# Optimization experiments

Measured on AMD Instinct MI355X. Metric: run time of the kernel, lower is better.

## Reference

```python
import jax, jax.numpy as jnp
import numpy as np

B, D, H = 8, 512, 8
HD = D // H            # 64 head dim
NS, NT = 8192, 4096    # search / template points
ATTN_EPS = 1e-6
LN_EPS = 1e-5


def layer_norm(x, g, b):
    m = jnp.mean(x, axis=-1, keepdims=True)
    v = jnp.mean((x - m) ** 2, axis=-1, keepdims=True)
    return (x - m) * jax.lax.rsqrt(v + LN_EPS) * g + b


def setup_inputs() -> dict:
    key = jax.random.key(0)
    ks = jax.random.split(key, 20)
    s = 0.02
    return {
        "search_feat": jax.random.normal(ks[0], (B, D, NS), jnp.float32),
        "search_xyz": jax.random.uniform(ks[1], (B, NS, 3), jnp.float32),
        "template_feat": jax.random.normal(ks[2], (B, D, NT), jnp.float32),
        "template_xyz": jax.random.uniform(ks[3], (B, NT, 3), jnp.float32),
        "pos_w1": jax.random.normal(ks[4], (3, D), jnp.float32) * s,
        "pos_b1": jnp.zeros((D,), jnp.float32),
        "pos_w2": jax.random.normal(ks[5], (D, D), jnp.float32) * s,
        "pos_b2": jnp.zeros((D,), jnp.float32),
        "wq": jax.random.normal(ks[6], (D, D), jnp.float32) * s,
        "wk": jax.random.normal(ks[7], (D, D), jnp.float32) * s,
        "wv": jax.random.normal(ks[8], (D, D), jnp.float32) * s,
        "w_merge": jax.random.normal(ks[9], (D, D), jnp.float32) * s,
        "mlp_w1": jax.random.normal(ks[10], (2 * D, 2 * D), jnp.float32) * s,
        "mlp_w2": jax.random.normal(ks[11], (2 * D, D), jnp.float32) * s,
        "ln1_g": jnp.ones((D,), jnp.float32),
        "ln1_b": jnp.zeros((D,), jnp.float32),
        "ln2_g": jnp.ones((D,), jnp.float32),
        "ln2_b": jnp.zeros((D,), jnp.float32),
    }


def reference(search_feat, search_xyz, template_feat, template_xyz,
              pos_w1, pos_b1, pos_w2, pos_b2, wq, wk, wv, w_merge,
              mlp_w1, mlp_w2, ln1_g, ln1_b, ln2_g, ln2_b):
    bs = search_feat.shape[0]
    sf = jnp.transpose(search_feat, (0, 2, 1))    # [B, Ns, D]
    tf = jnp.transpose(template_feat, (0, 2, 1))  # [B, Nt, D]

    # positional MLP on template coordinates
    pos = jax.nn.relu(template_xyz @ pos_w1 + pos_b1) @ pos_w2 + pos_b2
    tf_pos = tf + pos

    q = (sf @ wq).reshape(bs, NS, H, HD)
    k = (tf @ wk).reshape(bs, NT, H, HD)
    v = (tf_pos @ wv).reshape(bs, NT, H, HD)

    # LoFTR-style linear attention: phi(x) = elu(x) + 1
    Q = jax.nn.elu(q) + 1.0
    K = jax.nn.elu(k) + 1.0
    v_len = v.shape[1]
    v_n = v / v_len
    KV = jnp.einsum("bshd,bshv->bhdv", K, v_n)                 # [B,H,d,d]
    Z = 1.0 / (jnp.einsum("blhd,bhd->blh", Q, K.sum(axis=1)) + ATTN_EPS)
    msg = jnp.einsum("blhd,bhdv->blhv", Q, KV) * Z[..., None] * v_len

    msg = msg.reshape(bs, NS, H * HD) @ w_merge
    msg = layer_norm(msg, ln1_g, ln1_b)
    cat = jnp.concatenate([sf, msg], axis=2)                    # [B,Ns,2D]
    msg = jax.nn.relu(cat @ mlp_w1) @ mlp_w2
    msg = layer_norm(msg, ln2_g, ln2_b)
    return jnp.transpose(sf + msg, (0, 2, 1))                   # [B,D,Ns]
```

## Files before the change

### kernel.cpp

```cpp
#include <hip/hip_runtime.h>
#include <stdint.h>
#include <stddef.h>


using ushort_t = unsigned short;
using short8 = __attribute__((ext_vector_type(8))) short;
using f32x4  = __attribute__((ext_vector_type(4))) float;

#define DEVI __device__ __forceinline__

DEVI float b2f(unsigned short u) {
    unsigned v = ((unsigned)u) << 16;
    return __builtin_bit_cast(float, v);
}
DEVI unsigned short f2b(float x) {
    unsigned u = __builtin_bit_cast(unsigned, x);
    u += 0x7FFFu + ((u >> 16) & 1u);
    return (unsigned short)(u >> 16);
}
DEVI void gload16(const void* g, void* l) {
    __builtin_amdgcn_global_load_lds(
        (const __attribute__((address_space(1))) unsigned*)g,
        (__attribute__((address_space(3))) unsigned*)l, 16, 0, 0);
}

template <int EPI>
__global__ __launch_bounds__(512, 1)
void gemm_bf16(const ushort_t* __restrict__ A0, const ushort_t* __restrict__ A1,
               const ushort_t* __restrict__ Wt, ushort_t* __restrict__ C,
               const float* __restrict__ bias, const ushort_t* __restrict__ addm,
               int N, int K, int K0, int lda0, int lda1, int nn)
{
    __shared__ ushort_t As[3][128 * 64];
    __shared__ ushort_t Bs[3][256 * 64];
    const int tid = threadIdx.x;
    const int cpx = gridDim.x >> 3;
    const int lid = (blockIdx.x & 7) * cpx + (blockIdx.x >> 3);
    const int m0 = (lid / nn) * 128;
    const int n0 = (lid % nn) * 256;
    const int w = tid >> 6, l = tid & 63;
    const int wm = (w >> 2) * 64;
    const int wn = (w & 3) * 64;
    const int lr = l & 15, lg = l >> 4;
    const int str = tid >> 3;
    const int sc  = ((tid & 7) ^ (str & 7)) * 8;
    const int nk = K / 64;

    f32x4 acc[4][4] = {};

    auto stageA = [&](int kt, int buf) {
        const int kb = kt * 64;
        const ushort_t* asrc; int ld;
        if (kb < K0) { asrc = A0 + (size_t)m0 * lda0 + kb; ld = lda0; }
        else         { asrc = A1 + (size_t)m0 * lda1 + (kb - K0); ld = lda1; }
#pragma unroll
        for (int j = 0; j < 2; j++)
            gload16(asrc + (size_t)(j * 64 + str) * ld + sc,
                    (void*)(&As[buf][j * 4096] + tid * 8));
    };
    auto stageB = [&](int kt, int buf) {
        const int kb = kt * 64;
        const ushort_t* wsrc = Wt + (size_t)n0 * K + kb;
#pragma unroll
        for (int j = 0; j < 4; j++)
            gload16(wsrc + (size_t)(j * 64 + str) * K + sc,
                    (void*)(&Bs[buf][j * 4096] + tid * 8));
    };

    stageA(0, 0); stageB(0, 0);
    stageA(1, 1); stageB(1, 1);
    asm volatile("s_waitcnt vmcnt(6)" ::: "memory");
    __builtin_amdgcn_s_barrier();

    for (int t = 0; t < nk; ++t) {
        const int cur = t % 3;
        const int nxt = (t + 2) % 3;
        const bool pre = (t + 2) < nk;
        {
            short8 a[4], b[4];
#pragma unroll
            for (int mf = 0; mf < 4; mf++)
                a[mf] = *(const short8*)&As[cur][(wm + mf * 16 + lr) * 64 + ((lg) ^ (lr & 7)) * 8];
#pragma unroll
            for (int nf = 0; nf < 4; nf++)
                b[nf] = *(const short8*)&Bs[cur][(wn + nf * 16 + lr) * 64 + ((lg) ^ (lr & 7)) * 8];
            if (pre) stageA(t + 2, nxt);
            __builtin_amdgcn_s_setprio(1);
#pragma unroll
            for (int mf = 0; mf < 4; mf++)
#pragma unroll
                for (int nf = 0; nf < 4; nf++)
                    acc[mf][nf] = __builtin_amdgcn_mfma_f32_16x16x32_bf16(
                        a[mf], b[nf], acc[mf][nf], 0, 0, 0);
            __builtin_amdgcn_s_setprio(0);
        }
        {
            short8 a[4], b[4];
#pragma unroll
            for (int mf = 0; mf < 4; mf++)
                a[mf] = *(const short8*)&As[cur][(wm + mf * 16 + lr) * 64 + ((4 + lg) ^ (lr & 7)) * 8];
#pragma unroll
            for (int nf = 0; nf < 4; nf++)
                b[nf] = *(const short8*)&Bs[cur][(wn + nf * 16 + lr) * 64 + ((4 + lg) ^ (lr & 7)) * 8];
            if (pre) stageB(t + 2, nxt);
            __builtin_amdgcn_s_setprio(1);
#pragma unroll
            for (int mf = 0; mf < 4; mf++)
#pragma unroll
                for (int nf = 0; nf < 4; nf++)
                    acc[mf][nf] = __builtin_amdgcn_mfma_f32_16x16x32_bf16(
                        a[mf], b[nf], acc[mf][nf], 0, 0, 0);
            __builtin_amdgcn_s_setprio(0);
        }
        if (pre) { asm volatile("s_waitcnt vmcnt(6)" ::: "memory"); }
        else     { asm volatile("s_waitcnt vmcnt(0)" ::: "memory"); }
        __builtin_amdgcn_s_barrier();
    }

#pragma unroll
    for (int mf = 0; mf < 4; mf++) {
#pragma unroll
        for (int i = 0; i < 4; i++) {
            const int m = m0 + wm + mf * 16 + lg * 4 + i;
#pragma unroll
            for (int nf = 0; nf < 4; nf++) {
                const int n = n0 + wn + nf * 16 + lr;
                float x = acc[mf][nf][i];
                if constexpr (EPI == 1) { x = x > 0.f ? x + 1.f : __expf(x); }
                if constexpr (EPI == 2) { x += bias[n] + b2f(addm[(size_t)m * N + n]); }
                if constexpr (EPI == 3) { x = fmaxf(x, 0.f); }
                C[(size_t)m * N + n] = f2b(x);
            }
        }
    }
}

__global__ __launch_bounds__(256)
void transpose_f32_bf16(const float* __restrict__ in, ushort_t* __restrict__ out,
                        int R, int Cc)
{
    __shared__ float tile[64][65];
    const int t = threadIdx.x;
    const int c0 = blockIdx.x * 64, r0 = blockIdx.y * 64;
    const size_t bo = (size_t)blockIdx.z * (size_t)R * (size_t)Cc;
    const float* src = in + bo;
    ushort_t* dst = out + bo;
#pragma unroll
    for (int i = 0; i < 4; i++) {
        const int r = (t >> 4) + i * 16;
        const int c = (t & 15) * 4;
        const float4 v = *(const float4*)&src[(size_t)(r0 + r) * Cc + c0 + c];
        tile[r][c + 0] = v.x; tile[r][c + 1] = v.y;
        tile[r][c + 2] = v.z; tile[r][c + 3] = v.w;
    }
    __syncthreads();
#pragma unroll
    for (int i = 0; i < 2; i++) {
        const int c = (t >> 3) + i * 32;
        const int rs = (t & 7) * 8;
        short8 o;
#pragma unroll
        for (int j = 0; j < 8; j++) o[j] = (short)f2b(tile[rs + j][c]);
        *(short8*)&dst[(size_t)(c0 + c) * R + r0 + rs] = o;
    }
}

__global__ __launch_bounds__(256)
void pos_mlp1(const float* __restrict__ xyz, const float* __restrict__ w1,
              const float* __restrict__ b1, ushort_t* __restrict__ P1)
{
    const int t = threadIdx.x;
    const int m = blockIdx.x * 4 + (t >> 6);
    const int n0 = (t & 63) * 8;
    const float x = xyz[m * 3 + 0], y = xyz[m * 3 + 1], z = xyz[m * 3 + 2];
    short8 o;
#pragma unroll
    for (int j = 0; j < 8; j++) {
        const int n = n0 + j;
        float v = x * w1[n] + y * w1[512 + n] + z * w1[1024 + n] + b1[n];
        o[j] = (short)f2b(fmaxf(v, 0.f));
    }
    *(short8*)&P1[(size_t)m * 512 + n0] = o;
}

__global__ __launch_bounds__(256)
void kv_partial(const ushort_t* __restrict__ Kp, const ushort_t* __restrict__ V,
                float* __restrict__ KVp, float* __restrict__ Ksp)
{
    __shared__ ushort_t Ks[256 * 64];
    __shared__ ushort_t Vs[256 * 64];
    const int t = threadIdx.x;
    const int sp = blockIdx.x, h = blockIdx.y, b = blockIdx.z;
    const int d0 = t >> 2, e0 = (t & 3) * 16;
    const int srow = t >> 3, scol = (t & 7) * 8;
    float acc[16] = {};
    float ksum = 0.f;
    for (int c = 0; c < 4; c++) {
        if (c) __syncthreads();
        const size_t sbase = (size_t)b * 4096 + sp * 1024 + c * 256;
#pragma unroll
        for (int i = 0; i < 8; i++) {
            const size_t go = (sbase + i * 32 + srow) * 512 + h * 64 + scol;
            gload16(Kp + go, (void*)(&Ks[i * 2048] + t * 8));
            gload16(V + go, (void*)(&Vs[i * 2048] + t * 8));
        }
        __syncthreads();
        for (int s = 0; s < 256; s++) {
            const float k = b2f(Ks[s * 64 + d0]);
            if ((t & 3) == 0) ksum += k;
            const short8 v0 = *(const short8*)&Vs[s * 64 + e0];
            const short8 v1 = *(const short8*)&Vs[s * 64 + e0 + 8];
#pragma unroll
            for (int j = 0; j < 8; j++) {
                acc[j]     += k * b2f((unsigned short)v0[j]);
                acc[8 + j] += k * b2f((unsigned short)v1[j]);
            }
        }
    }
    const int bh = b * 8 + h;
    float* kvo = KVp + (((size_t)sp * 64 + bh) * 64 + d0) * 64 + e0;
#pragma unroll
    for (int j = 0; j < 16; j++) kvo[j] = acc[j];
    if ((t & 3) == 0) Ksp[((size_t)sp * 64 + bh) * 64 + d0] = ksum;
}

__global__ __launch_bounds__(256)
void kv_finalize(const float* __restrict__ KVp, const float* __restrict__ Ksp,
                 ushort_t* __restrict__ KVt)
{
    const int bh = blockIdx.x, t = threadIdx.x;
    ushort_t* o = KVt + (size_t)bh * 5120;
#pragma unroll
    for (int i = 0; i < 16; i++) {
        const int idx = i * 256 + t;
        const int e = idx >> 6, d = idx & 63;
        float s = 0.f;
#pragma unroll
        for (int sp = 0; sp < 4; sp++)
            s += KVp[(((size_t)sp * 64 + bh) * 64 + d) * 64 + e];
        o[idx] = f2b(s);
    }
    if (t < 64) {
        float s = 0.f;
#pragma unroll
        for (int sp = 0; sp < 4; sp++) s += Ksp[((size_t)sp * 64 + bh) * 64 + t];
        o[4096 + t] = f2b(s);
    }
    for (int idx = 4160 + t; idx < 5120; idx += 256) o[idx] = 0;
}

__global__ __launch_bounds__(256, 2)
void attn_apply(const ushort_t* __restrict__ Qp, const ushort_t* __restrict__ KVt,
                ushort_t* __restrict__ msg1)
{
    __shared__ ushort_t As[256 * 64];
    __shared__ ushort_t Bs[80 * 64];
    const int t = threadIdx.x;
    const int ch = blockIdx.x, h = blockIdx.y, b = blockIdx.z;
    const int w = t >> 6, l = t & 63;
    const int lr = l & 15, lg = l >> 4;
    const int row0 = ch * 256;
    const int srow = t >> 3;
    const int sc = ((t & 7) ^ (srow & 7)) * 8;
    const ushort_t* kv = KVt + (size_t)(b * 8 + h) * 5120;
#pragma unroll
    for (int i = 0; i < 2; i++)
        gload16(kv + (size_t)(i * 32 + srow) * 64 + sc,
                (void*)(&Bs[i * 2048] + t * 8));
    if (t < 128)
        gload16(kv + (size_t)(64 + srow) * 64 + sc,
                (void*)(&Bs[4096] + t * 8));
    const ushort_t* qb = Qp + ((size_t)b * 8192 + row0) * 512 + h * 64;
#pragma unroll
    for (int i = 0; i < 8; i++)
        gload16(qb + (size_t)(i * 32 + srow) * 512 + sc,
                (void*)(&As[i * 2048] + t * 8));
    __syncthreads();
    f32x4 acc[4][5] = {};
    const int wr = w * 64;
#pragma unroll
    for (int ks = 0; ks < 2; ks++) {
        const int kswz = ((ks * 4 + lg) ^ (lr & 7)) * 8;
        short8 a[4], bb[5];
#pragma unroll
        for (int mf = 0; mf < 4; mf++)
            a[mf] = *(const short8*)&As[(wr + mf * 16 + lr) * 64 + kswz];
#pragma unroll
        for (int nf = 0; nf < 5; nf++)
            bb[nf] = *(const short8*)&Bs[(nf * 16 + lr) * 64 + kswz];
#pragma unroll
        for (int mf = 0; mf < 4; mf++)
#pragma unroll
            for (int nf = 0; nf < 5; nf++)
                acc[mf][nf] = __builtin_amdgcn_mfma_f32_16x16x32_bf16(
                    a[mf], bb[nf], acc[mf][nf], 0, 0, 0);
    }
#pragma unroll
    for (int mf = 0; mf < 4; mf++) {
#pragma unroll
        for (int i = 0; i < 4; i++) {
            const int m = row0 + wr + mf * 16 + lg * 4 + i;
            const float zden = __shfl(acc[mf][4][i], (l & 48));
            const float z = 1.f / (zden + 1e-6f);
#pragma unroll
            for (int nf = 0; nf < 4; nf++) {
                const int e = nf * 16 + lr;
                msg1[((size_t)b * 8192 + m) * 512 + h * 64 + e] =
                    f2b(acc[mf][nf][i] * z);
            }
        }
    }
}

__global__ __launch_bounds__(256)
void layer_norm_k(ushort_t* __restrict__ X, const float* __restrict__ g,
                  const float* __restrict__ bta)
{
    const int t = threadIdx.x;
    const int row = blockIdx.x * 4 + (t >> 6);
    const int l = t & 63;
    ushort_t* x = X + (size_t)row * 512;
    const short8 v = *(const short8*)&x[l * 8];
    float f[8];
    float s = 0.f;
#pragma unroll
    for (int j = 0; j < 8; j++) { f[j] = b2f((unsigned short)v[j]); s += f[j]; }
#pragma unroll
    for (int o = 32; o > 0; o >>= 1) s += __shfl_xor(s, o);
    const float mean = s * (1.f / 512.f);
    float vs = 0.f;
#pragma unroll
    for (int j = 0; j < 8; j++) { const float d = f[j] - mean; vs += d * d; }
#pragma unroll
    for (int o = 32; o > 0; o >>= 1) vs += __shfl_xor(vs, o);
    const float rstd = rsqrtf(vs * (1.f / 512.f) + 1e-5f);
    short8 ov;
#pragma unroll
    for (int j = 0; j < 8; j++) {
        const int c = l * 8 + j;
        ov[j] = (short)f2b((f[j] - mean) * rstd * g[c] + bta[c]);
    }
    *(short8*)&x[l * 8] = ov;
}

__global__ __launch_bounds__(256)
void ln2_final(const ushort_t* __restrict__ outp, const ushort_t* __restrict__ sfT,
               const float* __restrict__ g, const float* __restrict__ bta,
               float* __restrict__ out)
{
    __shared__ ushort_t tile[64][514];
    const int t = threadIdx.x;
    const int ns0 = blockIdx.x * 64, b = blockIdx.y;
    const int w = t >> 6, l = t & 63;
#pragma unroll
    for (int rr = 0; rr < 16; rr++) {
        const int r = w * 16 + rr;
        const size_t grow = (size_t)b * 8192 + ns0 + r;
        const short8 v = *(const short8*)&outp[grow * 512 + l * 8];
        float f[8];
        float s = 0.f;
#pragma unroll
        for (int j = 0; j < 8; j++) { f[j] = b2f((unsigned short)v[j]); s += f[j]; }
#pragma unroll
        for (int o = 32; o > 0; o >>= 1) s += __shfl_xor(s, o);
        const float mean = s * (1.f / 512.f);
        float vs = 0.f;
#pragma unroll
        for (int j = 0; j < 8; j++) { const float d = f[j] - mean; vs += d * d; }
#pragma unroll
        for (int o = 32; o > 0; o >>= 1) vs += __shfl_xor(vs, o);
        const float rstd = rsqrtf(vs * (1.f / 512.f) + 1e-5f);
        const short8 sv = *(const short8*)&sfT[grow * 512 + l * 8];
        short8 ov;
#pragma unroll
        for (int j = 0; j < 8; j++) {
            const int c = l * 8 + j;
            ov[j] = (short)f2b(b2f((unsigned short)sv[j]) +
                               (f[j] - mean) * rstd * g[c] + bta[c]);
        }
        *(short8*)&tile[r][l * 8] = ov;
    }
    __syncthreads();
#pragma unroll
    for (int i = 0; i < 32; i++) {
        const int d = (t >> 4) + i * 16;
        const int nss = (t & 15) * 4;
        float4 o;
        o.x = b2f(tile[nss + 0][d]);
        o.y = b2f(tile[nss + 1][d]);
        o.z = b2f(tile[nss + 2][d]);
        o.w = b2f(tile[nss + 3][d]);
        *(float4*)&out[((size_t)b * 512 + d) * 8192 + ns0 + nss] = o;
    }
}

extern "C" void kernel_launch(void* const* d_in, const int* in_sizes, int n_in,
                              void* d_out, int out_size, void* d_ws, size_t ws_size,
                              hipStream_t stream)
{
    (void)in_sizes; (void)n_in; (void)out_size; (void)ws_size;
    const float* search_feat   = (const float*)d_in[0];
    const float* template_feat = (const float*)d_in[2];
    const float* template_xyz  = (const float*)d_in[3];
    const float* pos_w1  = (const float*)d_in[4];
    const float* pos_b1  = (const float*)d_in[5];
    const float* pos_w2  = (const float*)d_in[6];
    const float* pos_b2  = (const float*)d_in[7];
    const float* wq      = (const float*)d_in[8];
    const float* wk      = (const float*)d_in[9];
    const float* wv      = (const float*)d_in[10];
    const float* w_merge = (const float*)d_in[11];
    const float* mlp_w1  = (const float*)d_in[12];
    const float* mlp_w2  = (const float*)d_in[13];
    const float* ln1_g   = (const float*)d_in[14];
    const float* ln1_b   = (const float*)d_in[15];
    const float* ln2_g   = (const float*)d_in[16];
    const float* ln2_b   = (const float*)d_in[17];
    float* out = (float*)d_out;

    char* ws = (char*)d_ws;
    ushort_t* sfT    = (ushort_t*)(ws + 0);
    ushort_t* Qp     = (ushort_t*)(ws + 67108864);
    ushort_t* tfT    = (ushort_t*)(ws + 134217728);
    ushort_t* Kp     = (ushort_t*)(ws + 167772160);
    ushort_t* msg2   = (ushort_t*)(ws + 134217728);
    ushort_t* P1     = (ushort_t*)(ws + 201326592);
    ushort_t* Vv     = (ushort_t*)(ws + 201326592);
    ushort_t* tfpos  = (ushort_t*)(ws + 234881024);
    ushort_t* msg1   = (ushort_t*)(ws + 268435456);
    ushort_t* hidden = (ushort_t*)(ws + 201326592);
    ushort_t* outp   = Qp;
    ushort_t* wqT  = (ushort_t*)(ws + 335544320);
    ushort_t* wkT  = (ushort_t*)(ws + 336068608);
    ushort_t* wvT  = (ushort_t*)(ws + 336592896);
    ushort_t* wmT  = (ushort_t*)(ws + 337117184);
    ushort_t* pw2T = (ushort_t*)(ws + 337641472);
    ushort_t* w1T  = (ushort_t*)(ws + 338165760);
    ushort_t* w2T  = (ushort_t*)(ws + 340262912);
    float*    KVp  = (float*)(ws + 341311488);
    float*    Ksp  = (float*)(ws + 345505792);
    ushort_t* KVt  = (ushort_t*)(ws + 345571328);

    transpose_f32_bf16<<<dim3(128, 8, 8), 256, 0, stream>>>(search_feat, sfT, 512, 8192);
    transpose_f32_bf16<<<dim3(64, 8, 8), 256, 0, stream>>>(template_feat, tfT, 512, 4096);
    transpose_f32_bf16<<<dim3(8, 8, 1), 256, 0, stream>>>(wq, wqT, 512, 512);
    transpose_f32_bf16<<<dim3(8, 8, 1), 256, 0, stream>>>(wk, wkT, 512, 512);
    transpose_f32_bf16<<<dim3(8, 8, 1), 256, 0, stream>>>(wv, wvT, 512, 512);
    transpose_f32_bf16<<<dim3(8, 8, 1), 256, 0, stream>>>(w_merge, wmT, 512, 512);
    transpose_f32_bf16<<<dim3(8, 8, 1), 256, 0, stream>>>(pos_w2, pw2T, 512, 512);
    transpose_f32_bf16<<<dim3(16, 16, 1), 256, 0, stream>>>(mlp_w1, w1T, 1024, 1024);
    transpose_f32_bf16<<<dim3(8, 16, 1), 256, 0, stream>>>(mlp_w2, w2T, 1024, 512);

    gemm_bf16<1><<<dim3(1024), 512, 0, stream>>>(sfT, nullptr, wqT, Qp,
                                                 nullptr, nullptr, 512, 512, 512, 512, 0, 2);
    gemm_bf16<1><<<dim3(512), 512, 0, stream>>>(tfT, nullptr, wkT, Kp,
                                                nullptr, nullptr, 512, 512, 512, 512, 0, 2);
    pos_mlp1<<<dim3(8192), 256, 0, stream>>>(template_xyz, pos_w1, pos_b1, P1);
    gemm_bf16<2><<<dim3(512), 512, 0, stream>>>(P1, nullptr, pw2T, tfpos,
                                                pos_b2, tfT, 512, 512, 512, 512, 0, 2);
    gemm_bf16<0><<<dim3(512), 512, 0, stream>>>(tfpos, nullptr, wvT, Vv,
                                                nullptr, nullptr, 512, 512, 512, 512, 0, 2);
    kv_partial<<<dim3(4, 8, 8), 256, 0, stream>>>(Kp, Vv, KVp, Ksp);
    kv_finalize<<<dim3(64), 256, 0, stream>>>(KVp, Ksp, KVt);
    attn_apply<<<dim3(32, 8, 8), 256, 0, stream>>>(Qp, KVt, msg1);
    gemm_bf16<0><<<dim3(1024), 512, 0, stream>>>(msg1, nullptr, wmT, msg2,
                                                 nullptr, nullptr, 512, 512, 512, 512, 0, 2);
    layer_norm_k<<<dim3(16384), 256, 0, stream>>>(msg2, ln1_g, ln1_b);
    gemm_bf16<3><<<dim3(2048), 512, 0, stream>>>(sfT, msg2, w1T, hidden,
                                                 nullptr, nullptr, 1024, 1024, 512, 512, 512, 4);
    gemm_bf16<0><<<dim3(1024), 512, 0, stream>>>(hidden, nullptr, w2T, outp,
                                                 nullptr, nullptr, 512, 1024, 1024, 1024, 0, 2);
    ln2_final<<<dim3(128, 8), 256, 0, stream>>>(outp, sfT, ln2_g, ln2_b, out);
}
```

Baseline: 760.1 us.

## Enlarge GEMM tile to 256x256 with double-buffered ping-pong schedule

The bf16 GEMM tile grows from 128x256 to 256x256, and each wave now owns 128x64 outputs with 32 accumulators. The triple-buffered prefetch is replaced by double buffering with a barrier-interleaved schedule that splits LDS fragment loads, MFMA bursts and global staging across four sub-phases. Launch bounds are raised to allow two blocks per CU, and grid sizes are halved to match. The aim is more reuse per LDS load and better overlap of memory and MFMA work, at the cost of higher register pressure, 128KB of LDS per block (which may block two-block occupancy), many extra barriers, and fewer blocks for the smaller GEMMs.

After: 741.3 us. -2.5%, faster.

```diff
diff --git a/kernel.cpp b/kernel.cpp
--- a/kernel.cpp
+++ b/kernel.cpp
@@ -25,107 +25,113 @@
 }
 
 template <int EPI>
-__global__ __launch_bounds__(512, 1)
+__global__ __launch_bounds__(512, 2)
 void gemm_bf16(const ushort_t* __restrict__ A0, const ushort_t* __restrict__ A1,
                const ushort_t* __restrict__ Wt, ushort_t* __restrict__ C,
                const float* __restrict__ bias, const ushort_t* __restrict__ addm,
                int N, int K, int K0, int lda0, int lda1, int nn)
 {
-    __shared__ ushort_t As[3][128 * 64];
-    __shared__ ushort_t Bs[3][256 * 64];
+    __shared__ ushort_t As[2][256 * 64];
+    __shared__ ushort_t Bs[2][256 * 64];
     const int tid = threadIdx.x;
     const int cpx = gridDim.x >> 3;
     const int lid = (blockIdx.x & 7) * cpx + (blockIdx.x >> 3);
-    const int m0 = (lid / nn) * 128;
+    const int m0 = (lid / nn) * 256;
     const int n0 = (lid % nn) * 256;
     const int w = tid >> 6, l = tid & 63;
-    const int wm = (w >> 2) * 64;
+    const int wm = (w >> 2) * 128;
     const int wn = (w & 3) * 64;
     const int lr = l & 15, lg = l >> 4;
-    const int str = tid >> 3;
-    const int sc  = ((tid & 7) ^ (str & 7)) * 8;
+    const int srow = tid >> 3;
+    const int sck  = (tid & 7) ^ (srow & 7);
     const int nk = K / 64;
 
-    f32x4 acc[4][4] = {};
+    f32x4 acc[8][4] = {};
 
     auto stageA = [&](int kt, int buf) {
         const int kb = kt * 64;
-        const ushort_t* asrc; int ld;
-        if (kb < K0) { asrc = A0 + (size_t)m0 * lda0 + kb; ld = lda0; }
-        else         { asrc = A1 + (size_t)m0 * lda1 + (kb - K0); ld = lda1; }
-#pragma unroll
-        for (int j = 0; j < 2; j++)
-            gload16(asrc + (size_t)(j * 64 + str) * ld + sc,
+        const ushort_t* p; int ld;
+        if (kb < K0) { p = A0 + (size_t)m0 * lda0 + kb; ld = lda0; }
+        else         { p = A1 + (size_t)m0 * lda1 + (kb - K0); ld = lda1; }
+        p += (size_t)srow * ld + sck * 8;
+#pragma unroll
+        for (int j = 0; j < 4; j++)
+            gload16(p + (size_t)(j * 64) * ld,
                     (void*)(&As[buf][j * 4096] + tid * 8));
     };
     auto stageB = [&](int kt, int buf) {
-        const int kb = kt * 64;
-        const ushort_t* wsrc = Wt + (size_t)n0 * K + kb;
+        const ushort_t* p = Wt + (size_t)(n0 + srow) * K + kt * 64 + sck * 8;
 #pragma unroll
         for (int j = 0; j < 4; j++)
-            gload16(wsrc + (size_t)(j * 64 + str) * K + sc,
+            gload16(p + (size_t)(j * 64) * K,
                     (void*)(&Bs[buf][j * 4096] + tid * 8));
     };
 
     stageA(0, 0); stageB(0, 0);
-    stageA(1, 1); stageB(1, 1);
-    asm volatile("s_waitcnt vmcnt(6)" ::: "memory");
-    __builtin_amdgcn_s_barrier();
+    asm volatile("s_waitcnt vmcnt(0)" ::: "memory");
+    asm volatile("s_barrier" ::: "memory");
 
     for (int t = 0; t < nk; ++t) {
-        const int cur = t % 3;
-        const int nxt = (t + 2) % 3;
-        const bool pre = (t + 2) < nk;
-        {
-            short8 a[4], b[4];
+        const int cur = t & 1;
+        const bool pre = (t + 1) < nk;
+        short8 afr[4], bfr[4];
+
+        auto ldA = [&](int mh, int ks) {
+#pragma unroll
+            for (int mf = 0; mf < 4; mf++) {
+                const int r = wm + mh * 64 + mf * 16 + lr;
+                afr[mf] = *(const short8*)&As[cur][r * 64 + ((ks * 4 + lg) ^ (r & 7)) * 8];
+            }
+        };
+        auto ldB = [&](int ks) {
+#pragma unroll
+            for (int nf = 0; nf < 4; nf++) {
+                const int r = wn + nf * 16 + lr;
+                bfr[nf] = *(const short8*)&Bs[cur][r * 64 + ((ks * 4 + lg) ^ (r & 7)) * 8];
+            }
+        };
+        auto mm = [&](int mh) {
+            __builtin_amdgcn_s_setprio(1);
 #pragma unroll
             for (int mf = 0; mf < 4; mf++)
-                a[mf] = *(const short8*)&As[cur][(wm + mf * 16 + lr) * 64 + ((lg) ^ (lr & 7)) * 8];
-#pragma unroll
-            for (int nf = 0; nf < 4; nf++)
-                b[nf] = *(const short8*)&Bs[cur][(wn + nf * 16 + lr) * 64 + ((lg) ^ (lr & 7)) * 8];
-            if (pre) stageA(t + 2, nxt);
-            __builtin_amdgcn_s_setprio(1);
-#pragma unroll
-            for (int mf = 0; mf < 4; mf++)
 #pragma unroll
                 for (int nf = 0; nf < 4; nf++)
-                    acc[mf][nf] = __builtin_amdgcn_mfma_f32_16x16x32_bf16(
-                        a[mf], b[nf], acc[mf][nf], 0, 0, 0);
+                    acc[mh * 4 + mf][nf] = __builtin_amdgcn_mfma_f32_16x16x32_bf16(
+                        afr[mf], bfr[nf], acc[mh * 4 + mf][nf], 0, 0, 0);
             __builtin_amdgcn_s_setprio(0);
-        }
-        {
-            short8 a[4], b[4];
-#pragma unroll
-            for (int mf = 0; mf < 4; mf++)
-                a[mf] = *(const short8*)&As[cur][(wm + mf * 16 + lr) * 64 + ((4 + lg) ^ (lr & 7)) * 8];
-#pragma unroll
-            for (int nf = 0; nf < 4; nf++)
-                b[nf] = *(const short8*)&Bs[cur][(wn + nf * 16 + lr) * 64 + ((4 + lg) ^ (lr & 7)) * 8];
-            if (pre) stageB(t + 2, nxt);
-            __builtin_amdgcn_s_setprio(1);
-#pragma unroll
-            for (int mf = 0; mf < 4; mf++)
-#pragma unroll
-                for (int nf = 0; nf < 4; nf++)
-                    acc[mf][nf] = __builtin_amdgcn_mfma_f32_16x16x32_bf16(
-                        a[mf], b[nf], acc[mf][nf], 0, 0, 0);
-            __builtin_amdgcn_s_setprio(0);
-        }
-        if (pre) { asm volatile("s_waitcnt vmcnt(6)" ::: "memory"); }
-        else     { asm volatile("s_waitcnt vmcnt(0)" ::: "memory"); }
-        __builtin_amdgcn_s_barrier();
-    }
-
-#pragma unroll
-    for (int mf = 0; mf < 4; mf++) {
+        };
+
+        ldB(0); ldA(0, 0);
+        if (pre) stageA(t + 1, cur ^ 1);
+        asm volatile("s_barrier" ::: "memory");
+        mm(0);
+        asm volatile("s_barrier" ::: "memory");
+        ldA(1, 0);
+        if (pre) stageB(t + 1, cur ^ 1);
+        asm volatile("s_barrier" ::: "memory");
+        mm(1);
+        asm volatile("s_barrier" ::: "memory");
+        ldB(1); ldA(0, 1);
+        asm volatile("s_barrier" ::: "memory");
+        mm(0);
+        asm volatile("s_barrier" ::: "memory");
+        ldA(1, 1);
+        asm volatile("s_waitcnt vmcnt(0)" ::: "memory");
+        asm volatile("s_barrier" ::: "memory");
+        mm(1);
+        asm volatile("s_barrier" ::: "memory");
+    }
+
+#pragma unroll
+    for (int mi = 0; mi < 8; mi++) {
+        const int mh = mi >> 2, mf = mi & 3;
 #pragma unroll
         for (int i = 0; i < 4; i++) {
-            const int m = m0 + wm + mf * 16 + lg * 4 + i;
+            const int m = m0 + wm + mh * 64 + mf * 16 + lg * 4 + i;
 #pragma unroll
             for (int nf = 0; nf < 4; nf++) {
                 const int n = n0 + wn + nf * 16 + lr;
-                float x = acc[mf][nf][i];
+                float x = acc[mi][nf][i];
                 if constexpr (EPI == 1) { x = x > 0.f ? x + 1.f : __expf(x); }
                 if constexpr (EPI == 2) { x += bias[n] + b2f(addm[(size_t)m * N + n]); }
                 if constexpr (EPI == 3) { x = fmaxf(x, 0.f); }
@@ -451,24 +457,24 @@
     transpose_f32_bf16<<<dim3(16, 16, 1), 256, 0, stream>>>(mlp_w1, w1T, 1024, 1024);
     transpose_f32_bf16<<<dim3(8, 16, 1), 256, 0, stream>>>(mlp_w2, w2T, 1024, 512);
 
-    gemm_bf16<1><<<dim3(1024), 512, 0, stream>>>(sfT, nullptr, wqT, Qp,
-                                                 nullptr, nullptr, 512, 512, 512, 512, 0, 2);
-    gemm_bf16<1><<<dim3(512), 512, 0, stream>>>(tfT, nullptr, wkT, Kp,
+    gemm_bf16<1><<<dim3(512), 512, 0, stream>>>(sfT, nullptr, wqT, Qp,
+                                                nullptr, nullptr, 512, 512, 512, 512, 0, 2);
+    gemm_bf16<1><<<dim3(256), 512, 0, stream>>>(tfT, nullptr, wkT, Kp,
                                                 nullptr, nullptr, 512, 512, 512, 512, 0, 2);
     pos_mlp1<<<dim3(8192), 256, 0, stream>>>(template_xyz, pos_w1, pos_b1, P1);
-    gemm_bf16<2><<<dim3(512), 512, 0, stream>>>(P1, nullptr, pw2T, tfpos,
+    gemm_bf16<2><<<dim3(256), 512, 0, stream>>>(P1, nullptr, pw2T, tfpos,
                                                 pos_b2, tfT, 512, 512, 512, 512, 0, 2);
-    gemm_bf16<0><<<dim3(512), 512, 0, stream>>>(tfpos, nullptr, wvT, Vv,
+    gemm_bf16<0><<<dim3(256), 512, 0, stream>>>(tfpos, nullptr, wvT, Vv,
                                                 nullptr, nullptr, 512, 512, 512, 512, 0, 2);
     kv_partial<<<dim3(4, 8, 8), 256, 0, stream>>>(Kp, Vv, KVp, Ksp);
     kv_finalize<<<dim3(64), 256, 0, stream>>>(KVp, Ksp, KVt);
     attn_apply<<<dim3(32, 8, 8), 256, 0, stream>>>(Qp, KVt, msg1);
-    gemm_bf16<0><<<dim3(1024), 512, 0, stream>>>(msg1, nullptr, wmT, msg2,
-                                                 nullptr, nullptr, 512, 512, 512, 512, 0, 2);
+    gemm_bf16<0><<<dim3(512), 512, 0, stream>>>(msg1, nullptr, wmT, msg2,
+                                                nullptr, nullptr, 512, 512, 512, 512, 0, 2);
     layer_norm_k<<<dim3(16384), 256, 0, stream>>>(msg2, ln1_g, ln1_b);
-    gemm_bf16<3><<<dim3(2048), 512, 0, stream>>>(sfT, msg2, w1T, hidden,
+    gemm_bf16<3><<<dim3(1024), 512, 0, stream>>>(sfT, msg2, w1T, hidden,
                                                  nullptr, nullptr, 1024, 1024, 512, 512, 512, 4);
-    gemm_bf16<0><<<dim3(1024), 512, 0, stream>>>(hidden, nullptr, w2T, outp,
-                                                 nullptr, nullptr, 512, 1024, 1024, 1024, 0, 2);
+    gemm_bf16<0><<<dim3(512), 512, 0, stream>>>(hidden, nullptr, w2T, outp,
+                                                nullptr, nullptr, 512, 1024, 1024, 1024, 0, 2);
     ln2_final<<<dim3(128, 8), 256, 0, stream>>>(outp, sfT, ln2_g, ln2_b, out);
 }
```
